# Performance work log

Measured on AMD Instinct MI355X. Metric: run time of the kernel, lower is better.

## Reference

```python
import jax, jax.numpy as jnp
import numpy as np

EPS = 1e-5


def _rms_norm(x, w):
    # x: [..., C], w: [C]
    inv = jax.lax.rsqrt(jnp.mean(x * x, axis=-1, keepdims=True) + EPS)
    return x * inv * w


def setup_inputs() -> dict:
    key = jax.random.key(0)
    ks = jax.random.split(key, 8)
    N, H, C = 16384, 16, 32
    NE = 196608
    return {
        "q": jax.random.normal(ks[0], (N, H, C), dtype=jnp.float32),
        "k": jax.random.normal(ks[1], (N, H, C), dtype=jnp.float32),
        "v": jax.random.normal(ks[2], (N, H, C), dtype=jnp.float32),
        "e": jax.random.normal(ks[3], (NE, H, C), dtype=jnp.float32),
        "w_q_norm": jnp.ones((C,), dtype=jnp.float32),
        "w_k_norm": jnp.ones((C,), dtype=jnp.float32),
        "edge_src": jax.random.randint(ks[4], (NE,), 0, N, dtype=jnp.int32),
        "edge_dst": jax.random.randint(ks[5], (NE,), 0, N, dtype=jnp.int32),
    }


def reference(q, k, v, e, w_q_norm, w_k_norm, edge_src, edge_dst):
    N, H, C = q.shape
    qk_scale = 1.0 / np.sqrt(float(C))
    # fused QK RMSNorm (qk_norm == 1, elementwise_affine)
    qn = _rms_norm(q, w_q_norm)            # [N,H,C]
    kn = _rms_norm(k, w_k_norm)            # [N,H,C]
    ke = kn[edge_src] + e                  # [NE,H,C]
    ve = v[edge_src] + e                   # [NE,H,C]
    s = jnp.einsum("ehc,ehc->eh", qn[edge_dst], ke) * qk_scale  # [NE,H]
    # segment softmax over incoming edges per dst node
    m = jax.ops.segment_max(s, edge_dst, num_segments=N)        # [N,H]
    m = jnp.where(jnp.isfinite(m), m, 0.0)                      # empty rows -> 0 (matches kernel)
    alpha = jnp.exp(s - m[edge_dst])                            # [NE,H]
    denom = jax.ops.segment_sum(alpha, edge_dst, num_segments=N)            # [N,H]
    num = jax.ops.segment_sum(alpha[..., None] * ve, edge_dst, num_segments=N)  # [N,H,C]
    out = num / jnp.where(denom > 0, denom, 1.0)[..., None]
    return out
```

## Files before the change

kernel.cpp:

```cpp
#include <hip/hip_runtime.h>
#include <math.h>

#define H_DIM 16
#define C_DIM 32
#define EPSF 1e-5f

__device__ __forceinline__ float reduce8(float x) {
    x += __shfl_xor(x, 1);
    x += __shfl_xor(x, 2);
    x += __shfl_xor(x, 4);
    return x;
}

__global__ void zero_kernel(int* __restrict__ p, int n) {
    int i = blockIdx.x * blockDim.x + threadIdx.x;
    if (i < n) p[i] = 0;
}

__global__ void hist_kernel(const int* __restrict__ edst, int* __restrict__ counts, int ne) {
    int i = blockIdx.x * blockDim.x + threadIdx.x;
    if (i < ne) atomicAdd(&counts[edst[i]], 1);
}

__global__ __launch_bounds__(1024)
void scan_kernel(const int* __restrict__ counts, int* __restrict__ offsets, int n) {
    __shared__ int sdata[1024];
    __shared__ int carry_s;
    const int tid = threadIdx.x;
    if (tid == 0) { carry_s = 0; offsets[0] = 0; }
    __syncthreads();
    for (int base = 0; base < n; base += 1024) {
        int x = (base + tid < n) ? counts[base + tid] : 0;
        sdata[tid] = x;
        __syncthreads();
        for (int off = 1; off < 1024; off <<= 1) {
            int val = (tid >= off) ? sdata[tid - off] : 0;
            __syncthreads();
            sdata[tid] += val;
            __syncthreads();
        }
        int inc = sdata[tid];
        int carry = carry_s;
        if (base + tid < n) offsets[base + tid + 1] = carry + inc;
        __syncthreads();
        if (tid == 1023) carry_s = carry + inc;
        __syncthreads();
    }
}

__global__ void scatter_kernel(const int* __restrict__ esrc, const int* __restrict__ edst,
                               const int* __restrict__ offsets, int* __restrict__ cursor,
                               int* __restrict__ perm_eid, int* __restrict__ perm_src, int ne) {
    int i = blockIdx.x * blockDim.x + threadIdx.x;
    if (i < ne) {
        int d = edst[i];
        int pos = offsets[d] + atomicAdd(&cursor[d], 1);
        perm_eid[pos] = i;
        perm_src[pos] = esrc[i];
    }
}

__global__ __launch_bounds__(128)
void attn_kernel(const float* __restrict__ q, const float* __restrict__ k,
                 const float* __restrict__ v, const float* __restrict__ e,
                 const float* __restrict__ wq, const float* __restrict__ wk,
                 const int* __restrict__ offsets, const int* __restrict__ perm_eid,
                 const int* __restrict__ perm_src, float* __restrict__ out)
{
    const int node = blockIdx.x;
    const int t = threadIdx.x;
    const int h = t >> 3;
    const int c4 = (t & 7) << 2;
    const float qk_scale = 0.17677669529663687f;

    const size_t node_off = ((size_t)node * H_DIM + h) * C_DIM + c4;

    float4 qv = *(const float4*)(q + node_off);
    float qs = qv.x * qv.x + qv.y * qv.y + qv.z * qv.z + qv.w * qv.w;
    qs = reduce8(qs);
    float qinv = rsqrtf(qs * (1.0f / C_DIM) + EPSF);
    float4 wqv = *(const float4*)(wq + c4);
    float4 qn = make_float4(qv.x * qinv * wqv.x, qv.y * qinv * wqv.y,
                            qv.z * qinv * wqv.z, qv.w * qinv * wqv.w);
    float4 wkv = *(const float4*)(wk + c4);

    const int row0 = offsets[node];
    const int row1 = offsets[node + 1];

    float m = -INFINITY;
    float l = 0.0f;
    float4 acc = make_float4(0.f, 0.f, 0.f, 0.f);

    for (int j = row0; j < row1; ++j) {
        int eid = perm_eid[j];
        int src = perm_src[j];
        const size_t e_off = ((size_t)eid * H_DIM + h) * C_DIM + c4;
        const size_t s_off = ((size_t)src * H_DIM + h) * C_DIM + c4;
        float4 ev = *(const float4*)(e + e_off);
        float4 kv = *(const float4*)(k + s_off);
        float4 vv = *(const float4*)(v + s_off);

        float ks = kv.x * kv.x + kv.y * kv.y + kv.z * kv.z + kv.w * kv.w;
        ks = reduce8(ks);
        float kinv = rsqrtf(ks * (1.0f / C_DIM) + EPSF);
        float4 ke = make_float4(kv.x * kinv * wkv.x + ev.x,
                                kv.y * kinv * wkv.y + ev.y,
                                kv.z * kinv * wkv.z + ev.z,
                                kv.w * kinv * wkv.w + ev.w);

        float d = qn.x * ke.x + qn.y * ke.y + qn.z * ke.z + qn.w * ke.w;
        d = reduce8(d);
        float s = d * qk_scale;

        float mnew = fmaxf(m, s);
        float sc = __expf(m - mnew);
        float al = __expf(s - mnew);
        l = l * sc + al;
        acc.x = acc.x * sc + al * (vv.x + ev.x);
        acc.y = acc.y * sc + al * (vv.y + ev.y);
        acc.z = acc.z * sc + al * (vv.z + ev.z);
        acc.w = acc.w * sc + al * (vv.w + ev.w);
        m = mnew;
    }

    float invl = (l > 0.0f) ? (1.0f / l) : 0.0f;
    *(float4*)(out + node_off) = make_float4(acc.x * invl, acc.y * invl,
                                             acc.z * invl, acc.w * invl);
}

extern "C" void kernel_launch(void* const* d_in, const int* in_sizes, int n_in,
                              void* d_out, int out_size, void* d_ws, size_t ws_size,
                              hipStream_t stream) {
    const float* q  = (const float*)d_in[0];
    const float* k  = (const float*)d_in[1];
    const float* v  = (const float*)d_in[2];
    const float* e  = (const float*)d_in[3];
    const float* wq = (const float*)d_in[4];
    const float* wk = (const float*)d_in[5];
    const int* esrc = (const int*)d_in[6];
    const int* edst = (const int*)d_in[7];
    float* out = (float*)d_out;

    const int NE = in_sizes[6];
    const int C  = in_sizes[4];
    const int HC = in_sizes[3] / NE;
    const int N  = in_sizes[0] / HC;
    (void)C;

    int* wsp      = (int*)d_ws;
    int* counts   = wsp;
    int* cursor   = wsp + N;
    int* offsets  = wsp + 2 * N;
    int* perm_eid = wsp + 3 * N + 1;
    int* perm_src = perm_eid + NE;

    zero_kernel<<<(2 * N + 255) / 256, 256, 0, stream>>>(counts, 2 * N);
    hist_kernel<<<(NE + 255) / 256, 256, 0, stream>>>(edst, counts, NE);
    scan_kernel<<<1, 1024, 0, stream>>>(counts, offsets, N);
    scatter_kernel<<<(NE + 255) / 256, 256, 0, stream>>>(esrc, edst, offsets, cursor,
                                                         perm_eid, perm_src, NE);
    attn_kernel<<<N, 128, 0, stream>>>(q, k, v, e, wq, wk, offsets,
                                       perm_eid, perm_src, out);
}
```

Before: 702.5 us.

## Split per-node edge loop into two online-softmax streams, warp-shuffle scan, packed perm

The attention kernel now walks each node's incoming edges as two independent halves, each with its own online-softmax state, so two sets of gathered loads are in flight per iteration; the two partial results are merged at the end. The single-block scan replaces its shared-memory Hillis-Steele loop, which needed many barriers, with wave-level shuffle scans. Source and edge ids are packed into one int2 permutation array, so each edge needs a single index load. The cost is higher register pressure from the doubled accumulators and a small tail loop when the edge count is odd.

```diff
diff --git a/kernel.cpp b/kernel.cpp
--- a/kernel.cpp
+++ b/kernel.cpp
@@ -3,6 +3,7 @@
 
 #define H_DIM 16
 #define C_DIM 32
+#define HC_DIM (H_DIM * C_DIM)
 #define EPSF 1e-5f
 
 __device__ __forceinline__ float reduce8(float x) {
@@ -24,56 +25,91 @@
 
 __global__ __launch_bounds__(1024)
 void scan_kernel(const int* __restrict__ counts, int* __restrict__ offsets, int n) {
-    __shared__ int sdata[1024];
+    __shared__ int wsum[16];
     __shared__ int carry_s;
     const int tid = threadIdx.x;
+    const int lane = tid & 63;
+    const int wid = tid >> 6;
     if (tid == 0) { carry_s = 0; offsets[0] = 0; }
     __syncthreads();
     for (int base = 0; base < n; base += 1024) {
         int x = (base + tid < n) ? counts[base + tid] : 0;
-        sdata[tid] = x;
+        int v = x;
+        #pragma unroll
+        for (int off = 1; off < 64; off <<= 1) {
+            int y = __shfl_up(v, off);
+            if (lane >= off) v += y;
+        }
+        if (lane == 63) wsum[wid] = v;
         __syncthreads();
-        for (int off = 1; off < 1024; off <<= 1) {
-            int val = (tid >= off) ? sdata[tid - off] : 0;
-            __syncthreads();
-            sdata[tid] += val;
-            __syncthreads();
+        if (wid == 0 && lane < 16) {
+            int s = wsum[lane];
+            #pragma unroll
+            for (int off = 1; off < 16; off <<= 1) {
+                int y = __shfl_up(s, off);
+                if (lane >= off) s += y;
+            }
+            wsum[lane] = s;
         }
-        int inc = sdata[tid];
+        __syncthreads();
+        int waveoff = (wid == 0) ? 0 : wsum[wid - 1];
         int carry = carry_s;
-        if (base + tid < n) offsets[base + tid + 1] = carry + inc;
+        if (base + tid < n) offsets[base + tid + 1] = carry + waveoff + v;
         __syncthreads();
-        if (tid == 1023) carry_s = carry + inc;
+        if (tid == 1023) carry_s = carry + wsum[15];
         __syncthreads();
     }
 }
 
 __global__ void scatter_kernel(const int* __restrict__ esrc, const int* __restrict__ edst,
                                const int* __restrict__ offsets, int* __restrict__ cursor,
-                               int* __restrict__ perm_eid, int* __restrict__ perm_src, int ne) {
+                               int2* __restrict__ perm, int ne) {
     int i = blockIdx.x * blockDim.x + threadIdx.x;
     if (i < ne) {
         int d = edst[i];
         int pos = offsets[d] + atomicAdd(&cursor[d], 1);
-        perm_eid[pos] = i;
-        perm_src[pos] = esrc[i];
+        perm[pos] = make_int2(esrc[i], i);
     }
+}
+
+__device__ __forceinline__ void update_edge(float4 ev, float4 kv, float4 vv,
+                                            float4 qn, float4 wkv, float qk_scale,
+                                            float& m, float& l, float4& acc) {
+    float ks = kv.x * kv.x + kv.y * kv.y + kv.z * kv.z + kv.w * kv.w;
+    ks = reduce8(ks);
+    float kinv = rsqrtf(ks * (1.0f / C_DIM) + EPSF);
+    float kex = kv.x * kinv * wkv.x + ev.x;
+    float key = kv.y * kinv * wkv.y + ev.y;
+    float kez = kv.z * kinv * wkv.z + ev.z;
+    float kew = kv.w * kinv * wkv.w + ev.w;
+    float d = qn.x * kex + qn.y * key + qn.z * kez + qn.w * kew;
+    d = reduce8(d);
+    float s = d * qk_scale;
+    float mnew = fmaxf(m, s);
+    float sc = __expf(m - mnew);
+    float al = __expf(s - mnew);
+    l = l * sc + al;
+    acc.x = acc.x * sc + al * (vv.x + ev.x);
+    acc.y = acc.y * sc + al * (vv.y + ev.y);
+    acc.z = acc.z * sc + al * (vv.z + ev.z);
+    acc.w = acc.w * sc + al * (vv.w + ev.w);
+    m = mnew;
 }
 
 __global__ __launch_bounds__(128)
 void attn_kernel(const float* __restrict__ q, const float* __restrict__ k,
                  const float* __restrict__ v, const float* __restrict__ e,
                  const float* __restrict__ wq, const float* __restrict__ wk,
-                 const int* __restrict__ offsets, const int* __restrict__ perm_eid,
-                 const int* __restrict__ perm_src, float* __restrict__ out)
+                 const int* __restrict__ offsets, const int2* __restrict__ perm,
+                 float* __restrict__ out)
 {
     const int node = blockIdx.x;
     const int t = threadIdx.x;
-    const int h = t >> 3;
+    const int hc = t << 2;
     const int c4 = (t & 7) << 2;
     const float qk_scale = 0.17677669529663687f;
 
-    const size_t node_off = ((size_t)node * H_DIM + h) * C_DIM + c4;
+    const int node_off = node * HC_DIM + hc;
 
     float4 qv = *(const float4*)(q + node_off);
     float qs = qv.x * qv.x + qv.y * qv.y + qv.z * qv.z + qv.w * qv.w;
@@ -86,42 +122,44 @@
 
     const int row0 = offsets[node];
     const int row1 = offsets[node + 1];
+    const int len = row1 - row0;
+    const int mid = row0 + ((len + 1) >> 1);
 
-    float m = -INFINITY;
-    float l = 0.0f;
-    float4 acc = make_float4(0.f, 0.f, 0.f, 0.f);
+    float mA = -INFINITY, lA = 0.0f, mB = -INFINITY, lB = 0.0f;
+    float4 accA = make_float4(0.f, 0.f, 0.f, 0.f);
+    float4 accB = make_float4(0.f, 0.f, 0.f, 0.f);
 
-    for (int j = row0; j < row1; ++j) {
-        int eid = perm_eid[j];
-        int src = perm_src[j];
-        const size_t e_off = ((size_t)eid * H_DIM + h) * C_DIM + c4;
-        const size_t s_off = ((size_t)src * H_DIM + h) * C_DIM + c4;
-        float4 ev = *(const float4*)(e + e_off);
-        float4 kv = *(const float4*)(k + s_off);
-        float4 vv = *(const float4*)(v + s_off);
+    int jA = row0, jB = mid;
+    while (jA < mid && jB < row1) {
+        int2 pA = perm[jA];
+        int2 pB = perm[jB];
+        const float4 evA = *(const float4*)(e + (size_t)pA.y * HC_DIM + hc);
+        const float4 kvA = *(const float4*)(k + pA.x * HC_DIM + hc);
+        const float4 vvA = *(const float4*)(v + pA.x * HC_DIM + hc);
+        const float4 evB = *(const float4*)(e + (size_t)pB.y * HC_DIM + hc);
+        const float4 kvB = *(const float4*)(k + pB.x * HC_DIM + hc);
+        const float4 vvB = *(const float4*)(v + pB.x * HC_DIM + hc);
+        update_edge(evA, kvA, vvA, qn, wkv, qk_scale, mA, lA, accA);
+        update_edge(evB, kvB, vvB, qn, wkv, qk_scale, mB, lB, accB);
+        ++jA; ++jB;
+    }
+    while (jA < mid) {
+        int2 p = perm[jA];
+        const float4 ev = *(const float4*)(e + (size_t)p.y * HC_DIM + hc);
+        const float4 kv = *(const float4*)(k + p.x * HC_DIM + hc);
+        const float4 vv = *(const float4*)(v + p.x * HC_DIM + hc);
+        update_edge(ev, kv, vv, qn, wkv, qk_scale, mA, lA, accA);
+        ++jA;
+    }
 
-        float ks = kv.x * kv.x + kv.y * kv.y + kv.z * kv.z + kv.w * kv.w;
-        ks = reduce8(ks);
-        float kinv = rsqrtf(ks * (1.0f / C_DIM) + EPSF);
-        float4 ke = make_float4(kv.x * kinv * wkv.x + ev.x,
-                                kv.y * kinv * wkv.y + ev.y,
-                                kv.z * kinv * wkv.z + ev.z,
-                                kv.w * kinv * wkv.w + ev.w);
-
-        float d = qn.x * ke.x + qn.y * ke.y + qn.z * ke.z + qn.w * ke.w;
-        d = reduce8(d);
-        float s = d * qk_scale;
-
-        float mnew = fmaxf(m, s);
-        float sc = __expf(m - mnew);
-        float al = __expf(s - mnew);
-        l = l * sc + al;
-        acc.x = acc.x * sc + al * (vv.x + ev.x);
-        acc.y = acc.y * sc + al * (vv.y + ev.y);
-        acc.z = acc.z * sc + al * (vv.z + ev.z);
-        acc.w = acc.w * sc + al * (vv.w + ev.w);
-        m = mnew;
-    }
+    float M = fmaxf(mA, mB);
+    float fA = (lA > 0.0f) ? __expf(mA - M) : 0.0f;
+    float fB = (lB > 0.0f) ? __expf(mB - M) : 0.0f;
+    float l = lA * fA + lB * fB;
+    float4 acc = make_float4(accA.x * fA + accB.x * fB,
+                             accA.y * fA + accB.y * fB,
+                             accA.z * fA + accB.z * fB,
+                             accA.w * fA + accB.w * fB);
 
     float invl = (l > 0.0f) ? (1.0f / l) : 0.0f;
     *(float4*)(out + node_off) = make_float4(acc.x * invl, acc.y * invl,
@@ -142,23 +180,18 @@
     float* out = (float*)d_out;
 
     const int NE = in_sizes[6];
-    const int C  = in_sizes[4];
     const int HC = in_sizes[3] / NE;
     const int N  = in_sizes[0] / HC;
-    (void)C;
 
-    int* wsp      = (int*)d_ws;
-    int* counts   = wsp;
-    int* cursor   = wsp + N;
-    int* offsets  = wsp + 2 * N;
-    int* perm_eid = wsp + 3 * N + 1;
-    int* perm_src = perm_eid + NE;
+    int2* perm    = (int2*)d_ws;
+    int* counts   = (int*)(perm + NE);
+    int* cursor   = counts + N;
+    int* offsets  = cursor + N;
 
     zero_kernel<<<(2 * N + 255) / 256, 256, 0, stream>>>(counts, 2 * N);
     hist_kernel<<<(NE + 255) / 256, 256, 0, stream>>>(edst, counts, NE);
     scan_kernel<<<1, 1024, 0, stream>>>(counts, offsets, N);
     scatter_kernel<<<(NE + 255) / 256, 256, 0, stream>>>(esrc, edst, offsets, cursor,
-                                                         perm_eid, perm_src, NE);
-    attn_kernel<<<N, 128, 0, stream>>>(q, k, v, e, wq, wk, offsets,
-                                       perm_eid, perm_src, out);
+                                                         perm, NE);
+    attn_kernel<<<N, 128, 0, stream>>>(q, k, v, e, wq, wk, offsets, perm, out);
 }
```

After: 686.1 us. 1.02x faster.
